# Performance work log

Measured on AMD Instinct MI355X. Metric: run time of the kernel, lower is better.

Reference implementation:

```python
import jax, jax.numpy as jnp
import numpy as np

S, B, D = 2048, 2, 4096
H, KVH, HD = 32, 8, 128          # n_heads_q, n_kv_heads, head_dim
NREP = H // KVH                  # GQA repeat factor
ROPE_BASE = 10000.0


def _rope(x, cos, sin):
    # x: [B, S, h, HD]; cos/sin: [S, HD//2]
    xr = x.reshape(x.shape[:-1] + (-1, 2))
    x0, x1 = xr[..., 0], xr[..., 1]
    c = cos[None, :, None, :]
    s = sin[None, :, None, :]
    out = jnp.stack([x0 * c - x1 * s, x0 * s + x1 * c], axis=-1)
    return out.reshape(x.shape)


def setup_inputs() -> dict:
    key = jax.random.key(0)
    k0, k1, k2, k3, k4 = jax.random.split(key, 5)
    x = jax.random.normal(k0, (S, B, D), jnp.float32)
    inv_freq = 1.0 / (ROPE_BASE ** (np.arange(0, HD, 2, dtype=np.float64) / HD))  # [HD//2]
    t = np.arange(S, dtype=np.float64)[:, None] * inv_freq[None, :]               # [S, HD//2]
    freqs_cos = jnp.asarray(np.cos(t), jnp.float32)
    freqs_sin = jnp.asarray(np.sin(t), jnp.float32)
    scale = 0.02
    wq = jax.random.normal(k1, (H * HD, D), jnp.float32) * scale
    wk = jax.random.normal(k2, (KVH * HD, D), jnp.float32) * scale
    wv = jax.random.normal(k3, (KVH * HD, D), jnp.float32) * scale
    wo = jax.random.normal(k4, (D, H * HD), jnp.float32) * scale
    return {"x": x, "start_pos": 0, "freqs_cos": freqs_cos, "freqs_sin": freqs_sin,
            "wq": wq, "wk": wk, "wv": wv, "wo": wo}


def reference(x, start_pos, freqs_cos, freqs_sin, wq, wk, wv, wo):
    seq_len, batch, _ = x.shape
    # QKV projections (torch Linear: y = x @ W^T), then [S,B,*] -> [B,S,h,HD]
    q = (x @ wq.T).transpose(1, 0, 2).reshape(batch, seq_len, H, HD)
    k = (x @ wk.T).transpose(1, 0, 2).reshape(batch, seq_len, KVH, HD)
    v = (x @ wv.T).transpose(1, 0, 2).reshape(batch, seq_len, KVH, HD)
    # RoPE on q and k
    q = _rope(q, freqs_cos, freqs_sin)
    k = _rope(k, freqs_cos, freqs_sin)
    # repeat_kv (GQA)
    k = jnp.repeat(k, NREP, axis=2)
    v = jnp.repeat(v, NREP, axis=2)
    # [B, H, S, HD]
    q = q.transpose(0, 2, 1, 3)
    k = k.transpose(0, 2, 1, 3)
    v = v.transpose(0, 2, 1, 3)
    # causal scaled dot-product attention (SDPA is_causal=True equivalent)
    scores = jnp.einsum('bhqd,bhkd->bhqk', q, k) / np.float32(np.sqrt(HD))
    causal = jnp.tril(jnp.ones((seq_len, seq_len), dtype=bool))
    scores = jnp.where(causal[None, None], scores, jnp.float32(-jnp.inf))
    probs = jax.nn.softmax(scores.astype(jnp.float32), axis=-1).astype(q.dtype)
    out = jnp.einsum('bhqk,bhkd->bhqd', probs, v)
    # [B,H,S,HD] -> [B,S,H*HD] -> [S,B,H*HD]
    out = out.transpose(0, 2, 1, 3).reshape(batch, seq_len, H * HD).transpose(1, 0, 2)
    return out @ wo.T
```

## Files before the change

kernel.cpp:

```cpp
#include <hip/hip_runtime.h>

typedef __attribute__((ext_vector_type(8))) short s16x8;
typedef __attribute__((ext_vector_type(8))) __bf16 bf16x8;
typedef __attribute__((ext_vector_type(4))) float f32x4;

#define S_LEN 2048
#define KDIM  4096
#define CSOFT 0.12751743f

__device__ __forceinline__ unsigned short f2bf(float f) {
  unsigned u = __builtin_bit_cast(unsigned, f);
  u += 0x7fffu + ((u >> 16) & 1u);
  return (unsigned short)(u >> 16);
}

__device__ __forceinline__ f32x4 mfma_bf16(s16x8 a, s16x8 b, f32x4 c) {
  return __builtin_amdgcn_mfma_f32_16x16x32_bf16(
      __builtin_bit_cast(bf16x8, a), __builtin_bit_cast(bf16x8, b), c, 0, 0, 0);
}

__device__ __forceinline__ void gload_lds16(const unsigned short* g, void* l) {
  __builtin_amdgcn_global_load_lds(
      (const __attribute__((address_space(1))) void*)g,
      (__attribute__((address_space(3))) void*)l, 16, 0, 0);
}

__global__ void cvt_bf16(const float* __restrict__ in,
                         unsigned short* __restrict__ out, int n8) {
  int i = blockIdx.x * 256 + threadIdx.x;
  if (i >= n8) return;
  const float* p = in + (size_t)i * 8;
  f32x4 a = *(const f32x4*)(p);
  f32x4 b = *(const f32x4*)(p + 4);
  s16x8 v;
  v[0] = (short)f2bf(a[0]); v[1] = (short)f2bf(a[1]);
  v[2] = (short)f2bf(a[2]); v[3] = (short)f2bf(a[3]);
  v[4] = (short)f2bf(b[0]); v[5] = (short)f2bf(b[1]);
  v[6] = (short)f2bf(b[2]); v[7] = (short)f2bf(b[3]);
  *(s16x8*)(out + (size_t)i * 8) = v;
}

template <int EPI>
__global__ __launch_bounds__(512, 1)
void gemm256(const unsigned short* __restrict__ A,
             const unsigned short* __restrict__ B,
             void* __restrict__ Out,
             const float* __restrict__ cosT,
             const float* __restrict__ sinT) {
  const int K = KDIM;
  __shared__ __align__(16) unsigned short As[2 * 2 * 8192];
  __shared__ __align__(16) unsigned short Bs[2 * 2 * 8192];

  const int tid = threadIdx.x;
  const int lane = tid & 63, wid = tid >> 6;
  const int l15 = lane & 15, l4 = lane >> 4;
  const int wr = wid >> 2, wc = wid & 3;

  int bid = blockIdx.x;
  int wg = (bid & 7) * 32 + (bid >> 3);
  const int rt = wg >> 4, ct = wg & 15;
  const int row0 = rt * 256, col0 = ct * 256;

  const int ch0 = tid, ch1 = 512 + tid;
  const int sr0 = ch0 >> 3, u0 = (ch0 & 7) ^ (sr0 & 7);
  const int sr1 = ch1 >> 3, u1 = (ch1 & 7) ^ (sr1 & 7);
  const unsigned short* A0p = A + (size_t)(row0 + sr0) * K + u0 * 8;
  const unsigned short* A1p = A + (size_t)(row0 + sr1) * K + u1 * 8;
  const unsigned short* B0p = B + (size_t)(col0 + sr0) * K + u0 * 8;
  const unsigned short* B1p = B + (size_t)(col0 + sr1) * K + u1 * 8;

  const int rdo0 = l15 * 128 + ((l4 ^ (l15 & 7)) << 4);
  const int rdo1 = l15 * 128 + (((4 | l4) ^ (l15 & 7)) << 4);

  f32x4 acc[8][4];
#pragma unroll
  for (int m = 0; m < 8; m++)
#pragma unroll
    for (int n = 0; n < 4; n++) acc[m][n] = f32x4{0.f, 0.f, 0.f, 0.f};

  auto stageA = [&](int buf, int h, int kt) {
    char* d = (char*)As + buf * 32768 + h * 16384 + wid * 1024;
    size_t so = (size_t)h * 128 * K + kt;
    gload_lds16(A0p + so, d);
    gload_lds16(A1p + so, d + 8192);
  };
  auto stageB = [&](int buf, int h, int kt) {
    char* d = (char*)Bs + buf * 32768 + h * 16384 + wid * 1024;
    size_t so = (size_t)h * 128 * K + kt;
    gload_lds16(B0p + so, d);
    gload_lds16(B1p + so, d + 8192);
  };
  auto barsb = [&]() {
    __builtin_amdgcn_s_barrier();
    __builtin_amdgcn_sched_barrier(0);
  };

  stageA(0, 0, 0);
  stageA(0, 1, 0);
  stageB(0, 0, 0);
  stageB(0, 1, 0);
  stageA(1, 0, 64);
  asm volatile("s_waitcnt vmcnt(2)" ::: "memory");
  barsb();

  auto do_tile = [&](int tau, bool s123, bool s4, int vmend) {
    const int buf = tau & 1;
    const char* Ab = (const char*)As + buf * 32768 + wr * 16384;
    const char* Bb = (const char*)Bs + buf * 32768 + (wc >> 1) * 16384 +
                     (wc & 1) * 8192;
    const int kt1 = (tau + 1) * 64, kt2 = (tau + 2) * 64;
    s16x8 af0[4], af1[4], bA0[2], bA1[2], bB0[2], bB1[2];

#pragma unroll
    for (int mi = 0; mi < 4; mi++) {
      af0[mi] = *(const s16x8*)(Ab + mi * 2048 + rdo0);
      af1[mi] = *(const s16x8*)(Ab + mi * 2048 + rdo1);
    }
#pragma unroll
    for (int ni = 0; ni < 2; ni++) {
      bA0[ni] = *(const s16x8*)(Bb + ni * 2048 + rdo0);
      bA1[ni] = *(const s16x8*)(Bb + ni * 2048 + rdo1);
    }
    if (s123) stageA(buf ^ 1, 1, kt1);
    barsb();
    __builtin_amdgcn_s_setprio(1);
#pragma unroll
    for (int mi = 0; mi < 4; mi++)
#pragma unroll
      for (int ni = 0; ni < 2; ni++) {
        acc[mi][ni] = mfma_bf16(af0[mi], bA0[ni], acc[mi][ni]);
        acc[mi][ni] = mfma_bf16(af1[mi], bA1[ni], acc[mi][ni]);
      }
    __builtin_amdgcn_s_setprio(0);
    barsb();

#pragma unroll
    for (int ni = 0; ni < 2; ni++) {
      bB0[ni] = *(const s16x8*)(Bb + (2 + ni) * 2048 + rdo0);
      bB1[ni] = *(const s16x8*)(Bb + (2 + ni) * 2048 + rdo1);
    }
    if (s123) stageB(buf ^ 1, 0, kt1);
    barsb();
    __builtin_amdgcn_s_setprio(1);
#pragma unroll
    for (int mi = 0; mi < 4; mi++)
#pragma unroll
      for (int ni = 0; ni < 2; ni++) {
        acc[mi][2 + ni] = mfma_bf16(af0[mi], bB0[ni], acc[mi][2 + ni]);
        acc[mi][2 + ni] = mfma_bf16(af1[mi], bB1[ni], acc[mi][2 + ni]);
      }
    __builtin_amdgcn_s_setprio(0);
    barsb();

#pragma unroll
    for (int mi = 0; mi < 4; mi++) {
      af0[mi] = *(const s16x8*)(Ab + 8192 + mi * 2048 + rdo0);
      af1[mi] = *(const s16x8*)(Ab + 8192 + mi * 2048 + rdo1);
    }
    if (s123) stageB(buf ^ 1, 1, kt1);
    barsb();
    __builtin_amdgcn_s_setprio(1);
#pragma unroll
    for (int mi = 0; mi < 4; mi++)
#pragma unroll
      for (int ni = 0; ni < 2; ni++) {
        acc[4 + mi][2 + ni] = mfma_bf16(af0[mi], bB0[ni], acc[4 + mi][2 + ni]);
        acc[4 + mi][2 + ni] = mfma_bf16(af1[mi], bB1[ni], acc[4 + mi][2 + ni]);
      }
    __builtin_amdgcn_s_setprio(0);
    barsb();

    if (s4) stageA(buf, 0, kt2);
    barsb();
    __builtin_amdgcn_s_setprio(1);
#pragma unroll
    for (int mi = 0; mi < 4; mi++)
#pragma unroll
      for (int ni = 0; ni < 2; ni++) {
        acc[4 + mi][ni] = mfma_bf16(af0[mi], bA0[ni], acc[4 + mi][ni]);
        acc[4 + mi][ni] = mfma_bf16(af1[mi], bA1[ni], acc[4 + mi][ni]);
      }
    __builtin_amdgcn_s_setprio(0);
    if (vmend == 2) {
      asm volatile("s_waitcnt vmcnt(2)" ::: "memory");
    } else if (vmend == 0) {
      asm volatile("s_waitcnt vmcnt(0)" ::: "memory");
    }
    barsb();
  };

  for (int tau = 0; tau < 62; tau++) do_tile(tau, true, true, 2);
  do_tile(62, true, false, 0);
  do_tile(63, false, false, -1);

#pragma unroll
  for (int m = 0; m < 8; m++) {
#pragma unroll
    for (int n = 0; n < 4; n++) {
      f32x4 v = acc[m][n];
      int rowb = row0 + wr * 128 + m * 16 + l4 * 4;
      int col = col0 + wc * 64 + n * 16 + l15;
      if (EPI == 3) {
        float* o = (float*)Out;
#pragma unroll
        for (int r = 0; r < 4; r++) o[(size_t)(rowb + r) * 4096 + col] = v[r];
      } else {
        float vp[4];
#pragma unroll
        for (int r = 0; r < 4; r++) vp[r] = __shfl_xor(v[r], 1, 64);
        bool odd = lane & 1;
        int fi = (col & 127) >> 1;
#pragma unroll
        for (int r = 0; r < 4; r++) {
          int nn = rowb + r, s = nn >> 1;
          float c = cosT[s * 64 + fi], sn = sinT[s * 64 + fi];
          v[r] = odd ? (vp[r] * sn + v[r] * c) : (v[r] * c - vp[r] * sn);
        }
        unsigned short* o = (unsigned short*)Out;
        int hh = col >> 7, hd = col & 127;
#pragma unroll
        for (int r = 0; r < 4; r++) {
          int nn = rowb + r, s = nn >> 1, b = nn & 1;
          o[((size_t)(b * 32 + hh) * 2048 + s) * 128 + hd] = f2bf(v[r]);
        }
      }
    }
  }
}

template <int EPI, int N, bool B_FP32>
__global__ __launch_bounds__(256, 2)
void gemm_bt(const unsigned short* __restrict__ A,
             const float* __restrict__ Bw32,
             const unsigned short* __restrict__ Bw16,
             void* __restrict__ Out,
             const float* __restrict__ cosT,
             const float* __restrict__ sinT) {
  const int K = KDIM;
  const int tid = threadIdx.x;
  const int lane = tid & 63, wid = tid >> 6;
  const int l15 = lane & 15, l4 = lane >> 4;
  const int nct = N / 128;
  const int ct = blockIdx.x % nct, rt = blockIdx.x / nct;
  const int row0 = rt * 128, col0 = ct * 128;
  const int wr = wid >> 1, wc = wid & 1;

  __shared__ __align__(16) unsigned short As[128 * 32];
  __shared__ __align__(16) unsigned short Bs[128 * 32];

  f32x4 acc[4][4];
#pragma unroll
  for (int i = 0; i < 4; i++)
#pragma unroll
    for (int j = 0; j < 4; j++) acc[i][j] = f32x4{0.f, 0.f, 0.f, 0.f};

  for (int kt = 0; kt < K; kt += 32) {
#pragma unroll
    for (int i = 0; i < 2; i++) {
      int j = wid * 2 + i;
      int ch = j * 64 + lane;
      int r = ch >> 2, c = ch & 3;
      int sc = c ^ ((r >> 1) & 3);
      gload_lds16(A + (size_t)(row0 + r) * K + kt + sc * 8, (char*)As + j * 1024);
    }
    if (B_FP32) {
#pragma unroll
      for (int j = 0; j < 2; j++) {
        int ch = tid + 256 * j;
        int r = ch >> 2, c = ch & 3;
        const float* src = Bw32 + (size_t)(col0 + r) * K + kt + c * 8;
        f32x4 f0 = *(const f32x4*)(src);
        f32x4 f1 = *(const f32x4*)(src + 4);
        s16x8 v;
        v[0] = (short)f2bf(f0[0]); v[1] = (short)f2bf(f0[1]);
        v[2] = (short)f2bf(f0[2]); v[3] = (short)f2bf(f0[3]);
        v[4] = (short)f2bf(f1[0]); v[5] = (short)f2bf(f1[1]);
        v[6] = (short)f2bf(f1[2]); v[7] = (short)f2bf(f1[3]);
        int sw = c ^ ((r >> 1) & 3);
        *(s16x8*)((char*)Bs + r * 64 + sw * 16) = v;
      }
    } else {
#pragma unroll
      for (int i = 0; i < 2; i++) {
        int j = wid * 2 + i;
        int ch = j * 64 + lane;
        int r = ch >> 2, c = ch & 3;
        int sc = c ^ ((r >> 1) & 3);
        gload_lds16(Bw16 + (size_t)(col0 + r) * K + kt + sc * 8, (char*)Bs + j * 1024);
      }
    }
    __syncthreads();

    s16x8 af[4], bfr[4];
#pragma unroll
    for (int mi = 0; mi < 4; mi++) {
      int r = wr * 64 + mi * 16 + l15;
      int sw = l4 ^ ((r >> 1) & 3);
      af[mi] = *(const s16x8*)((char*)As + r * 64 + sw * 16);
    }
#pragma unroll
    for (int ni = 0; ni < 4; ni++) {
      int r = wc * 64 + ni * 16 + l15;
      int sw = l4 ^ ((r >> 1) & 3);
      bfr[ni] = *(const s16x8*)((char*)Bs + r * 64 + sw * 16);
    }
#pragma unroll
    for (int mi = 0; mi < 4; mi++)
#pragma unroll
      for (int ni = 0; ni < 4; ni++)
        acc[mi][ni] = mfma_bf16(af[mi], bfr[ni], acc[mi][ni]);
    __syncthreads();
  }

#pragma unroll
  for (int mi = 0; mi < 4; mi++) {
#pragma unroll
    for (int ni = 0; ni < 4; ni++) {
      f32x4 v = acc[mi][ni];
      int rowb = row0 + wr * 64 + mi * 16 + l4 * 4;
      int col = col0 + wc * 64 + ni * 16 + l15;
      if (EPI == 3) {
        float* o = (float*)Out;
#pragma unroll
        for (int r = 0; r < 4; r++) o[(size_t)(rowb + r) * 4096 + col] = v[r];
      } else {
        if (EPI != 2) {
          float vp[4];
#pragma unroll
          for (int r = 0; r < 4; r++) vp[r] = __shfl_xor(v[r], 1, 64);
          bool odd = lane & 1;
          int fi = (col & 127) >> 1;
#pragma unroll
          for (int r = 0; r < 4; r++) {
            int n = rowb + r, s = n >> 1;
            float c = cosT[s * 64 + fi], sn = sinT[s * 64 + fi];
            v[r] = odd ? (vp[r] * sn + v[r] * c) : (v[r] * c - vp[r] * sn);
          }
        }
        unsigned short* o = (unsigned short*)Out;
        int hh = col >> 7, hd = col & 127;
#pragma unroll
        for (int r = 0; r < 4; r++) {
          int n = rowb + r, s = n >> 1, b = n & 1;
          size_t idx;
          if (EPI == 0)      idx = ((size_t)(b * 32 + hh) * 2048 + s) * 128 + hd;
          else if (EPI == 1) idx = ((size_t)(b * 8 + hh) * 2048 + s) * 128 + hd;
          else               idx = ((size_t)(b * 8 + hh) * 128 + hd) * 2048 + s;
          o[idx] = f2bf(v[r]);
        }
      }
    }
  }
}

__global__ __launch_bounds__(256, 2)
void attn_fwd(const unsigned short* __restrict__ Qa,
              const unsigned short* __restrict__ Ka,
              const unsigned short* __restrict__ Vt,
              unsigned short* __restrict__ AO) {
  int bid = blockIdx.x;
  int pid = bid & 7;
  int h = (bid >> 3) & 31;
  int b = bid >> 8;
  int kvh = h >> 2;
  int tid = threadIdx.x, lane = tid & 63, wid = tid >> 6;
  int l15 = lane & 15, l4 = lane >> 4;

  __shared__ __align__(16) unsigned short Ks[64 * 128];
  __shared__ __align__(16) unsigned short Vs[128 * 64];
  __shared__ __align__(16) unsigned short Ps[4][32 * 64];

  const unsigned short* Qp = Qa + ((size_t)(b * 32 + h) * 2048) * 128;
  const unsigned short* Kp = Ka + ((size_t)(b * 8 + kvh) * 2048) * 128;
  const unsigned short* Vp = Vt + ((size_t)(b * 8 + kvh) * 128) * 2048;

  for (int half = 0; half < 2; half++) {
    int qt = half == 0 ? (7 - pid) : (8 + pid);
    int q0 = qt * 128, qr0 = q0 + wid * 32;

    s16x8 qf[2][4];
#pragma unroll
    for (int mi = 0; mi < 2; mi++)
#pragma unroll
      for (int ks = 0; ks < 4; ks++)
        qf[mi][ks] = *(const s16x8*)(Qp + (size_t)(qr0 + mi * 16 + l15) * 128 +
                                     ks * 32 + l4 * 8);

    f32x4 o[2][8];
#pragma unroll
    for (int mi = 0; mi < 2; mi++)
#pragma unroll
      for (int nb = 0; nb < 8; nb++) o[mi][nb] = f32x4{0.f, 0.f, 0.f, 0.f};
    float m[2][4], lsum[2][4];
#pragma unroll
    for (int mi = 0; mi < 2; mi++)
#pragma unroll
      for (int pr = 0; pr < 4; pr++) { m[mi][pr] = -1e30f; lsum[mi][pr] = 0.f; }

    int nt = q0 / 64 + 2;
    for (int t = 0; t < nt; t++) {
      int s0 = t * 64;
      const unsigned short* ktp = Kp + (size_t)s0 * 128;
#pragma unroll
      for (int i = 0; i < 4; i++) {
        int j = wid * 4 + i;
        int ch = j * 64 + lane;
        {
          int r = ch >> 4, cl = ch & 15;
          int sc = (cl & 8) | ((cl ^ (r & 7)) & 7);
          gload_lds16(ktp + r * 128 + sc * 8, (char*)Ks + j * 1024);
        }
        {
          int r = ch >> 3, p = ch & 7;
          int sc = p ^ (r & 7);
          gload_lds16(Vp + (size_t)r * 2048 + s0 + sc * 8, (char*)Vs + j * 1024);
        }
      }
      __syncthreads();

      if (s0 <= qr0 + 31) {
        f32x4 sc[2][4];
#pragma unroll
        for (int mi = 0; mi < 2; mi++)
#pragma unroll
          for (int kb = 0; kb < 4; kb++) sc[mi][kb] = f32x4{0.f, 0.f, 0.f, 0.f};
#pragma unroll
        for (int kb = 0; kb < 4; kb++) {
          int r = kb * 16 + l15;
#pragma unroll
          for (int ks = 0; ks < 4; ks++) {
            int c = ks * 4 + l4;
            int sw = (c & 8) | ((c ^ (r & 7)) & 7);
            s16x8 kf = *(const s16x8*)((char*)Ks + r * 256 + sw * 16);
            sc[0][kb] = mfma_bf16(qf[0][ks], kf, sc[0][kb]);
            sc[1][kb] = mfma_bf16(qf[1][ks], kf, sc[1][kb]);
          }
        }
        bool needmask = (s0 + 63) > qr0;
#pragma unroll
        for (int mi = 0; mi < 2; mi++) {
          if (needmask) {
#pragma unroll
            for (int kb = 0; kb < 4; kb++) {
              int kg = s0 + kb * 16 + l15;
#pragma unroll
              for (int pr = 0; pr < 4; pr++) {
                int qg = qr0 + mi * 16 + l4 * 4 + pr;
                if (kg > qg) sc[mi][kb][pr] = -1e30f;
              }
            }
          }
          float rm[4];
#pragma unroll
          for (int pr = 0; pr < 4; pr++)
            rm[pr] = fmaxf(fmaxf(sc[mi][0][pr], sc[mi][1][pr]),
                           fmaxf(sc[mi][2][pr], sc[mi][3][pr]));
#pragma unroll
          for (int xm = 1; xm <= 8; xm <<= 1)
#pragma unroll
            for (int pr = 0; pr < 4; pr++)
              rm[pr] = fmaxf(rm[pr], __shfl_xor(rm[pr], xm, 64));
          bool grow = false;
#pragma unroll
          for (int pr = 0; pr < 4; pr++)
            grow = grow || ((rm[pr] - m[mi][pr]) * CSOFT > 8.f);
          if (__any(grow)) {
            float fac[4];
#pragma unroll
            for (int pr = 0; pr < 4; pr++) {
              float nm = fmaxf(m[mi][pr], rm[pr]);
              fac[pr] = __builtin_amdgcn_exp2f((m[mi][pr] - nm) * CSOFT);
              m[mi][pr] = nm;
              lsum[mi][pr] *= fac[pr];
            }
#pragma unroll
            for (int nb = 0; nb < 8; nb++)
#pragma unroll
              for (int pr = 0; pr < 4; pr++) o[mi][nb][pr] *= fac[pr];
          }
          float rs[4] = {0.f, 0.f, 0.f, 0.f};
#pragma unroll
          for (int kb = 0; kb < 4; kb++)
#pragma unroll
            for (int pr = 0; pr < 4; pr++) {
              float p = __builtin_amdgcn_exp2f((sc[mi][kb][pr] - m[mi][pr]) * CSOFT);
              sc[mi][kb][pr] = p;
              rs[pr] += p;
            }
#pragma unroll
          for (int xm = 1; xm <= 8; xm <<= 1)
#pragma unroll
            for (int pr = 0; pr < 4; pr++) rs[pr] += __shfl_xor(rs[pr], xm, 64);
#pragma unroll
          for (int pr = 0; pr < 4; pr++) lsum[mi][pr] += rs[pr];
          char* pb = (char*)(&Ps[wid][0]);
#pragma unroll
          for (int kb = 0; kb < 4; kb++) {
            int col = kb * 16 + l15;
#pragma unroll
            for (int pr = 0; pr < 4; pr++) {
              int row = mi * 16 + l4 * 4 + pr;
              *(unsigned short*)(pb + row * 128 + (((col >> 3) ^ (row & 7)) * 16) +
                                 (col & 7) * 2) = f2bf(sc[mi][kb][pr]);
            }
          }
        }
        char* pb = (char*)(&Ps[wid][0]);
#pragma unroll
        for (int ks = 0; ks < 2; ks++) {
          s16x8 pa[2];
#pragma unroll
          for (int mi = 0; mi < 2; mi++) {
            int row = mi * 16 + l15;
            int c = ks * 4 + l4;
            pa[mi] = *(const s16x8*)(pb + row * 128 + ((c ^ (row & 7)) * 16));
          }
#pragma unroll
          for (int nb = 0; nb < 8; nb++) {
            int r = nb * 16 + l15;
            int c = ks * 4 + l4;
            s16x8 vf = *(const s16x8*)((char*)Vs + r * 128 + ((c ^ (r & 7)) * 16));
            o[0][nb] = mfma_bf16(pa[0], vf, o[0][nb]);
            o[1][nb] = mfma_bf16(pa[1], vf, o[1][nb]);
          }
        }
      }
      __syncthreads();
    }

#pragma unroll
    for (int mi = 0; mi < 2; mi++) {
      float inv[4];
#pragma unroll
      for (int pr = 0; pr < 4; pr++) inv[pr] = 1.f / lsum[mi][pr];
#pragma unroll
      for (int nb = 0; nb < 8; nb++) {
        int col = h * 128 + nb * 16 + l15;
#pragma unroll
        for (int pr = 0; pr < 4; pr++) {
          int q = qr0 + mi * 16 + l4 * 4 + pr;
          AO[(size_t)(q * 2 + b) * 4096 + col] = f2bf(o[mi][nb][pr] * inv[pr]);
        }
      }
    }
  }
}

extern "C" void kernel_launch(void* const* d_in, const int* in_sizes, int n_in,
                              void* d_out, int out_size, void* d_ws, size_t ws_size,
                              hipStream_t stream) {
  const float* x = (const float*)d_in[0];
  const float* cosT = (const float*)d_in[2];
  const float* sinT = (const float*)d_in[3];
  const float* wq = (const float*)d_in[4];
  const float* wk = (const float*)d_in[5];
  const float* wv = (const float*)d_in[6];
  const float* wo = (const float*)d_in[7];
  float* out = (float*)d_out;

  char* ws = (char*)d_ws;
  unsigned short* xb = (unsigned short*)(ws);
  unsigned short* Qa = (unsigned short*)(ws + 33554432ull);
  unsigned short* Ka = (unsigned short*)(ws + 67108864ull);
  unsigned short* Vt = (unsigned short*)(ws + 75497472ull);
  unsigned short* AO = (unsigned short*)(ws + 83886080ull);
  unsigned short* wqb = (unsigned short*)(ws + 117440512ull);
  unsigned short* wkb = (unsigned short*)(ws + 150994944ull);
  unsigned short* wvb = (unsigned short*)(ws + 159383552ull);
  unsigned short* wob = (unsigned short*)(ws + 167772160ull);
  bool wcvt = ws_size >= 201326592ull;

  cvt_bf16<<<8192, 256, 0, stream>>>(x, xb, 2097152);
  if (wcvt) {
    cvt_bf16<<<8192, 256, 0, stream>>>(wq, wqb, 2097152);
    cvt_bf16<<<2048, 256, 0, stream>>>(wk, wkb, 524288);
    cvt_bf16<<<2048, 256, 0, stream>>>(wv, wvb, 524288);
    cvt_bf16<<<8192, 256, 0, stream>>>(wo, wob, 2097152);
    gemm256<0><<<256, 512, 0, stream>>>(xb, wqb, Qa, cosT, sinT);
    gemm_bt<1, 1024, false><<<256, 256, 0, stream>>>(xb, nullptr, wkb, Ka, cosT, sinT);
    gemm_bt<2, 1024, false><<<256, 256, 0, stream>>>(xb, nullptr, wvb, Vt, cosT, sinT);
  } else {
    gemm_bt<0, 4096, true><<<1024, 256, 0, stream>>>(xb, wq, nullptr, Qa, cosT, sinT);
    gemm_bt<1, 1024, true><<<256, 256, 0, stream>>>(xb, wk, nullptr, Ka, cosT, sinT);
    gemm_bt<2, 1024, true><<<256, 256, 0, stream>>>(xb, wv, nullptr, Vt, cosT, sinT);
  }
  attn_fwd<<<512, 256, 0, stream>>>(Qa, Ka, Vt, AO);
  if (wcvt) {
    gemm256<3><<<256, 512, 0, stream>>>(AO, wob, out, cosT, sinT);
  } else {
    gemm_bt<3, 4096, true><<<1024, 256, 0, stream>>>(AO, wo, nullptr, out, cosT, sinT);
  }
}
```

Measured before the change: 620.1 us.

## Restructure GEMM main loop into four-quadrant schedule with deeper A prefetch

Rewrites the 256x256 GEMM inner loop so each K tile loads all A and B fragments for both halves into registers once, then runs four MFMA quadrants, each with its own global-to-LDS prefetch slot. A is now prefetched two tiles ahead, both of its halves, while B is one tile ahead, and the wait count is relaxed to vmcnt(4). The intent is to hide more global latency and cut repeated LDS fragment reads. It costs more registers for the extra fragment arrays and relies on correct buffer reuse ordering with the barriers.

```diff
diff --git a/kernel.cpp b/kernel.cpp
--- a/kernel.cpp
+++ b/kernel.cpp
@@ -90,108 +90,103 @@
     gload_lds16(B0p + so, d);
     gload_lds16(B1p + so, d + 8192);
   };
-  auto barsb = [&]() {
+  auto bar = [&]() {
     __builtin_amdgcn_s_barrier();
     __builtin_amdgcn_sched_barrier(0);
   };
+  auto quad = [&](const s16x8* ak0, const s16x8* ak1,
+                  const s16x8* bk0, const s16x8* bk1, int mb, int nb) {
+    __builtin_amdgcn_s_setprio(1);
+#pragma unroll
+    for (int mi = 0; mi < 4; mi++)
+#pragma unroll
+      for (int ni = 0; ni < 2; ni++) {
+        acc[mb + mi][nb + ni] =
+            mfma_bf16(ak0[mi], bk0[ni], acc[mb + mi][nb + ni]);
+        acc[mb + mi][nb + ni] =
+            mfma_bf16(ak1[mi], bk1[ni], acc[mb + mi][nb + ni]);
+      }
+    __builtin_amdgcn_s_setprio(0);
+  };
+
+  auto tile4 = [&](int buf, auto st1, auto st2, auto st3, auto st4,
+                   int vmEnd) {
+    const char* Ab = (const char*)As + buf * 32768 + wr * 16384;
+    const char* Bb = (const char*)Bs + buf * 32768 + (wc >> 1) * 16384 +
+                     (wc & 1) * 8192;
+    s16x8 a0k0[4], a0k1[4], a1k0[4], a1k1[4];
+    s16x8 b0k0[2], b0k1[2], b1k0[2], b1k1[2];
+
+#pragma unroll
+    for (int mi = 0; mi < 4; mi++) {
+      a0k0[mi] = *(const s16x8*)(Ab + mi * 2048 + rdo0);
+      a0k1[mi] = *(const s16x8*)(Ab + mi * 2048 + rdo1);
+    }
+#pragma unroll
+    for (int ni = 0; ni < 2; ni++) {
+      b0k0[ni] = *(const s16x8*)(Bb + ni * 2048 + rdo0);
+      b0k1[ni] = *(const s16x8*)(Bb + ni * 2048 + rdo1);
+    }
+    st1();
+    bar();
+    quad(a0k0, a0k1, b0k0, b0k1, 0, 0);
+    bar();
+
+#pragma unroll
+    for (int mi = 0; mi < 4; mi++) {
+      a1k0[mi] = *(const s16x8*)(Ab + 8192 + mi * 2048 + rdo0);
+      a1k1[mi] = *(const s16x8*)(Ab + 8192 + mi * 2048 + rdo1);
+    }
+#pragma unroll
+    for (int ni = 0; ni < 2; ni++) {
+      b1k0[ni] = *(const s16x8*)(Bb + 4096 + ni * 2048 + rdo0);
+      b1k1[ni] = *(const s16x8*)(Bb + 4096 + ni * 2048 + rdo1);
+    }
+    st2();
+    bar();
+    quad(a1k0, a1k1, b0k0, b0k1, 4, 0);
+    bar();
+
+    st3();
+    bar();
+    quad(a0k0, a0k1, b1k0, b1k1, 0, 2);
+    bar();
+
+    st4();
+    bar();
+    quad(a1k0, a1k1, b1k0, b1k1, 4, 2);
+    if (vmEnd == 4) {
+      asm volatile("s_waitcnt vmcnt(4)" ::: "memory");
+    } else if (vmEnd == 0) {
+      asm volatile("s_waitcnt vmcnt(0)" ::: "memory");
+    }
+    bar();
+  };
+  auto nop = [&]() {};
 
   stageA(0, 0, 0);
   stageA(0, 1, 0);
   stageB(0, 0, 0);
   stageB(0, 1, 0);
   stageA(1, 0, 64);
-  asm volatile("s_waitcnt vmcnt(2)" ::: "memory");
-  barsb();
-
-  auto do_tile = [&](int tau, bool s123, bool s4, int vmend) {
-    const int buf = tau & 1;
-    const char* Ab = (const char*)As + buf * 32768 + wr * 16384;
-    const char* Bb = (const char*)Bs + buf * 32768 + (wc >> 1) * 16384 +
-                     (wc & 1) * 8192;
-    const int kt1 = (tau + 1) * 64, kt2 = (tau + 2) * 64;
-    s16x8 af0[4], af1[4], bA0[2], bA1[2], bB0[2], bB1[2];
-
-#pragma unroll
-    for (int mi = 0; mi < 4; mi++) {
-      af0[mi] = *(const s16x8*)(Ab + mi * 2048 + rdo0);
-      af1[mi] = *(const s16x8*)(Ab + mi * 2048 + rdo1);
-    }
-#pragma unroll
-    for (int ni = 0; ni < 2; ni++) {
-      bA0[ni] = *(const s16x8*)(Bb + ni * 2048 + rdo0);
-      bA1[ni] = *(const s16x8*)(Bb + ni * 2048 + rdo1);
-    }
-    if (s123) stageA(buf ^ 1, 1, kt1);
-    barsb();
-    __builtin_amdgcn_s_setprio(1);
-#pragma unroll
-    for (int mi = 0; mi < 4; mi++)
-#pragma unroll
-      for (int ni = 0; ni < 2; ni++) {
-        acc[mi][ni] = mfma_bf16(af0[mi], bA0[ni], acc[mi][ni]);
-        acc[mi][ni] = mfma_bf16(af1[mi], bA1[ni], acc[mi][ni]);
-      }
-    __builtin_amdgcn_s_setprio(0);
-    barsb();
-
-#pragma unroll
-    for (int ni = 0; ni < 2; ni++) {
-      bB0[ni] = *(const s16x8*)(Bb + (2 + ni) * 2048 + rdo0);
-      bB1[ni] = *(const s16x8*)(Bb + (2 + ni) * 2048 + rdo1);
-    }
-    if (s123) stageB(buf ^ 1, 0, kt1);
-    barsb();
-    __builtin_amdgcn_s_setprio(1);
-#pragma unroll
-    for (int mi = 0; mi < 4; mi++)
-#pragma unroll
-      for (int ni = 0; ni < 2; ni++) {
-        acc[mi][2 + ni] = mfma_bf16(af0[mi], bB0[ni], acc[mi][2 + ni]);
-        acc[mi][2 + ni] = mfma_bf16(af1[mi], bB1[ni], acc[mi][2 + ni]);
-      }
-    __builtin_amdgcn_s_setprio(0);
-    barsb();
-
-#pragma unroll
-    for (int mi = 0; mi < 4; mi++) {
-      af0[mi] = *(const s16x8*)(Ab + 8192 + mi * 2048 + rdo0);
-      af1[mi] = *(const s16x8*)(Ab + 8192 + mi * 2048 + rdo1);
-    }
-    if (s123) stageB(buf ^ 1, 1, kt1);
-    barsb();
-    __builtin_amdgcn_s_setprio(1);
-#pragma unroll
-    for (int mi = 0; mi < 4; mi++)
-#pragma unroll
-      for (int ni = 0; ni < 2; ni++) {
-        acc[4 + mi][2 + ni] = mfma_bf16(af0[mi], bB0[ni], acc[4 + mi][2 + ni]);
-        acc[4 + mi][2 + ni] = mfma_bf16(af1[mi], bB1[ni], acc[4 + mi][2 + ni]);
-      }
-    __builtin_amdgcn_s_setprio(0);
-    barsb();
-
-    if (s4) stageA(buf, 0, kt2);
-    barsb();
-    __builtin_amdgcn_s_setprio(1);
-#pragma unroll
-    for (int mi = 0; mi < 4; mi++)
-#pragma unroll
-      for (int ni = 0; ni < 2; ni++) {
-        acc[4 + mi][ni] = mfma_bf16(af0[mi], bA0[ni], acc[4 + mi][ni]);
-        acc[4 + mi][ni] = mfma_bf16(af1[mi], bA1[ni], acc[4 + mi][ni]);
-      }
-    __builtin_amdgcn_s_setprio(0);
-    if (vmend == 2) {
-      asm volatile("s_waitcnt vmcnt(2)" ::: "memory");
-    } else if (vmend == 0) {
-      asm volatile("s_waitcnt vmcnt(0)" ::: "memory");
-    }
-    barsb();
-  };
-
-  for (int tau = 0; tau < 62; tau++) do_tile(tau, true, true, 2);
-  do_tile(62, true, false, 0);
-  do_tile(63, false, false, -1);
+  stageA(1, 1, 64);
+  asm volatile("s_waitcnt vmcnt(4)" ::: "memory");
+  bar();
+
+  for (int j = 0; j < 31; j++) {
+    const int k1 = (2 * j + 1) * 64, k2 = (2 * j + 2) * 64,
+              k3 = (2 * j + 3) * 64;
+    tile4(0, [&] { stageB(1, 0, k1); }, [&] { stageB(1, 1, k1); },
+          [&] { stageA(0, 0, k2); }, [&] { stageA(0, 1, k2); }, 4);
+    tile4(1, [&] { stageB(0, 0, k2); }, [&] { stageB(0, 1, k2); },
+          [&] { stageA(1, 0, k3); }, [&] { stageA(1, 1, k3); }, 4);
+  }
+  {
+    const int k1 = 63 * 64;
+    tile4(0, [&] { stageB(1, 0, k1); }, [&] { stageB(1, 1, k1); }, nop, nop,
+          0);
+    tile4(1, nop, nop, nop, nop, -1);
+  }
 
 #pragma unroll
   for (int m = 0; m < 8; m++) {
```

Result: no change. 626.4 us (+1.0%).
